# Performance work log

Measured on AMD Instinct MI355X. Metric: run time of the kernel, lower is better.

## Reference

```python
import jax, jax.numpy as jnp
import numpy as np

SEQ = 64  # hard-coded by tf.tile multiples=[1, 64, 1]


def setup_inputs() -> dict:
    key = jax.random.key(0)
    k1, k2, k3, k4 = jax.random.split(key, 4)
    B, V, D = 1024, 300, 512
    return {
        "word_ids_en": jax.random.randint(k1, (B, SEQ), 0, V, dtype=jnp.int32),
        "word_ids_fr": jax.random.randint(k2, (B, SEQ), 0, V, dtype=jnp.int32),
        "emb_kernel": jax.random.normal(k3, (V, D), dtype=jnp.float32) * 0.05,
        "Qdense": jax.random.normal(k4, (D, D), dtype=jnp.float32) * 0.05,
    }


def reference(word_ids_en, word_ids_fr, emb_kernel, Qdense):
    # Encoder side (French)
    embedded_fr = emb_kernel[word_ids_fr]                      # [B, S, D]
    mask_fr = (word_ids_fr != 0).astype(jnp.float32)           # [B, S]
    # Q = K = V = x @ W (same weight, three identical projections in source)
    qkv = jnp.einsum('bsd,de->bse', embedded_fr, Qdense)       # [B, S, D]
    # scores = Q K^T, masked multiplicatively along the key axis (no softmax)
    scores = jnp.einsum('bqd,bkd->bqk', qkv, qkv) * mask_fr[:, None, :]  # [B, S, S]
    encoded = jnp.einsum('bqk,bkd->bqd', scores, qkv)          # [B, S, D]
    # Decoder side (English) + residual add
    embedded_en = emb_kernel[word_ids_en]                      # [B, S, D]
    return embedded_en + encoded
```

## Files before the change

### kernel.cpp

```cpp
#include <hip/hip_runtime.h>
#include <hip/hip_bf16.h>

#define SEQ 64
#define DIM 512
#define VOCAB 300
#define LDQ 516
#define LDSC 72

typedef __attribute__((ext_vector_type(8))) short short8;
typedef __attribute__((ext_vector_type(4))) float floatx4;

static __device__ inline unsigned short f2bf(float x) {
    __hip_bfloat16 t = __float2bfloat16(x);
    return *reinterpret_cast<unsigned short*>(&t);
}

static __device__ inline short8 ld8(const unsigned short* p) {
    union { short8 s; uint2 u[2]; } r;
    r.u[0] = *(const uint2*)p;
    r.u[1] = *(const uint2*)(p + 4);
    return r.s;
}

__global__ __launch_bounds__(64) void proj_kernel(
    const float* __restrict__ emb,
    const float* __restrict__ Q,
    __hip_bfloat16* __restrict__ P)
{
    const int lane = threadIdx.x & 63;
    const int quad = lane >> 4;
    const int l16 = lane & 15;
    const int nt = blockIdx.x;
    const int mt = blockIdx.y;
    const int n = nt * 16 + l16;
    const int vrow = mt * 16 + l16;

    floatx4 acc = {};
#pragma unroll 4
    for (int k0 = 0; k0 < DIM; k0 += 32) {
        float4 x0 = {0, 0, 0, 0}, x1 = {0, 0, 0, 0};
        if (vrow < VOCAB) {
            x0 = *(const float4*)(emb + (size_t)vrow * DIM + k0 + quad * 8);
            x1 = *(const float4*)(emb + (size_t)vrow * DIM + k0 + quad * 8 + 4);
        }
        union { short8 s; unsigned short h[8]; } ua;
        ua.h[0] = f2bf(x0.x); ua.h[1] = f2bf(x0.y); ua.h[2] = f2bf(x0.z); ua.h[3] = f2bf(x0.w);
        ua.h[4] = f2bf(x1.x); ua.h[5] = f2bf(x1.y); ua.h[6] = f2bf(x1.z); ua.h[7] = f2bf(x1.w);

        union { short8 s; unsigned short h[8]; } ub;
#pragma unroll
        for (int j = 0; j < 8; j++)
            ub.h[j] = f2bf(Q[(size_t)(k0 + quad * 8 + j) * DIM + n]);

        acc = __builtin_amdgcn_mfma_f32_16x16x32_bf16(ua.s, ub.s, acc, 0, 0, 0);
    }
#pragma unroll
    for (int r = 0; r < 4; r++) {
        int v = mt * 16 + quad * 4 + r;
        if (v < VOCAB) P[(size_t)v * DIM + n] = __float2bfloat16(acc[r]);
    }
}

__global__ __launch_bounds__(512, 4) void fused_attn_kernel(
    const int* __restrict__ ids_en,
    const int* __restrict__ ids_fr,
    const float* __restrict__ emb,
    const __hip_bfloat16* __restrict__ P,
    float* __restrict__ out)
{
    __shared__ __align__(16) unsigned short qk[SEQ * LDQ];
    __shared__ __align__(16) unsigned short sc[SEQ * LDSC];

    const int b = blockIdx.x;
    const int tid = threadIdx.x;
    const int lane = tid & 63;
    const int w = tid >> 6;
    const int quad = lane >> 4;
    const int l16 = lane & 15;
    const int wv = __builtin_amdgcn_readfirstlane(w);

    {
        int rid[8];
#pragma unroll
        for (int i = 0; i < 8; i++)
            rid[i] = ids_fr[b * SEQ + i * 8 + wv];
        uint4 v[8];
#pragma unroll
        for (int i = 0; i < 8; i++)
            v[i] = *(const uint4*)(P + (size_t)rid[i] * DIM + lane * 8);
#pragma unroll
        for (int i = 0; i < 8; i++) {
            unsigned short* dst = qk + (i * 8 + wv) * LDQ + lane * 8;
            *(uint2*)dst = make_uint2(v[i].x, v[i].y);
            *(uint2*)(dst + 4) = make_uint2(v[i].z, v[i].w);
        }
    }

    const int t0 = w * 2;
    const int qi = w >> 1;
    const int ki0 = t0 & 3, ki1 = (t0 + 1) & 3;
    float mk0 = (ids_fr[b * SEQ + ki0 * 16 + l16] != 0) ? 1.0f : 0.0f;
    float mk1 = (ids_fr[b * SEQ + ki1 * 16 + l16] != 0) ? 1.0f : 0.0f;
    int idE[4];
#pragma unroll
    for (int q = 0; q < 4; q++)
        idE[q] = ids_en[b * SEQ + q * 16 + l16];

    __syncthreads();

    short8 bbr[2][4];
    {
        floatx4 accS[2] = {};
        for (int k0 = 0; k0 < DIM; k0 += 32) {
            short8 aa = ld8(qk + (qi * 16 + l16) * LDQ + k0 + quad * 8);
            short8 b0 = ld8(qk + (ki0 * 16 + l16) * LDQ + k0 + quad * 8);
            accS[0] = __builtin_amdgcn_mfma_f32_16x16x32_bf16(aa, b0, accS[0], 0, 0, 0);
            short8 b1 = ld8(qk + (ki1 * 16 + l16) * LDQ + k0 + quad * 8);
            accS[1] = __builtin_amdgcn_mfma_f32_16x16x32_bf16(aa, b1, accS[1], 0, 0, 0);
        }

#pragma unroll
        for (int kx = 0; kx < 2; kx++)
#pragma unroll
            for (int ni = 0; ni < 4; ni++)
#pragma unroll
                for (int j = 0; j < 8; j++)
                    ((unsigned short*)&bbr[kx][ni])[j] =
                        qk[(kx * 32 + quad * 8 + j) * LDQ + w * 64 + ni * 16 + l16];

#pragma unroll
        for (int r = 0; r < 4; r++) {
            int row = qi * 16 + quad * 4 + r;
            sc[row * LDSC + ki0 * 16 + l16] = f2bf(accS[0][r] * mk0);
            sc[row * LDSC + ki1 * 16 + l16] = f2bf(accS[1][r] * mk1);
        }
    }
    __syncthreads();

    const size_t out_base = (size_t)b * SEQ * DIM;
#pragma unroll
    for (int p = 0; p < 2; p++) {
        floatx4 acc[2][4] = {};
#pragma unroll
        for (int kx = 0; kx < 2; kx++) {
            short8 bf_[2];
#pragma unroll
            for (int mi = 0; mi < 2; mi++)
                bf_[mi] = *(const short8*)(
                    sc + (p * 32 + mi * 16 + l16) * LDSC + kx * 32 + quad * 8);
#pragma unroll
            for (int ni = 0; ni < 4; ni++)
#pragma unroll
                for (int mi = 0; mi < 2; mi++)
                    acc[mi][ni] = __builtin_amdgcn_mfma_f32_16x16x32_bf16(
                        bbr[kx][ni], bf_[mi], acc[mi][ni], 0, 0, 0);
        }

#pragma unroll
        for (int mi = 0; mi < 2; mi++) {
            int m = p * 32 + mi * 16 + l16;
            floatx4 e[4];
#pragma unroll
            for (int ni = 0; ni < 4; ni++)
                e[ni] = *(const floatx4*)(
                    emb + (size_t)idE[p * 2 + mi] * DIM + w * 64 + ni * 16 + quad * 4);
#pragma unroll
            for (int ni = 0; ni < 4; ni++) {
                floatx4 o = e[ni] + acc[mi][ni];
                *(floatx4*)(out + out_base + (size_t)m * DIM + w * 64 + ni * 16 + quad * 4) = o;
            }
        }
    }
}

extern "C" void kernel_launch(void* const* d_in, const int* in_sizes, int n_in,
                              void* d_out, int out_size, void* d_ws, size_t ws_size,
                              hipStream_t stream) {
    const int* ids_en = (const int*)d_in[0];
    const int* ids_fr = (const int*)d_in[1];
    const float* emb  = (const float*)d_in[2];
    const float* Qd   = (const float*)d_in[3];
    float* out = (float*)d_out;

    const int B = in_sizes[0] / SEQ;

    __hip_bfloat16* P = (__hip_bfloat16*)d_ws;

    proj_kernel<<<dim3(32, 19), 64, 0, stream>>>(emb, Qd, P);
    fused_attn_kernel<<<B, 512, 0, stream>>>(ids_en, ids_fr, emb, P, out);
}
```

Measured before the change: 181.3 us.

## Stage output through LDS for coalesced stores; use direct global-to-LDS gather

The gather of projected rows into LDS now uses global_load_lds (direct global-to-LDS DMA) instead of going through registers. The output GEMM operands are swapped so each wave's accumulator tile is written into the reused qk LDS buffer as fp32. The tile is then re-read row-contiguously, the embedding residual is added, and full rows are written with nontemporal stores. This aims to make the global writes and the emb reads fully coalesced, at the cost of extra LDS traffic and added __syncthreads barriers per output pass.

```diff
diff --git a/kernel.cpp b/kernel.cpp
--- a/kernel.cpp
+++ b/kernel.cpp
@@ -20,6 +20,12 @@
     r.u[0] = *(const uint2*)p;
     r.u[1] = *(const uint2*)(p + 4);
     return r.s;
+}
+
+static __device__ inline void gload_lds16(const void* g, void* l) {
+    __builtin_amdgcn_global_load_lds(
+        (const __attribute__((address_space(1))) void*)g,
+        (__attribute__((address_space(3))) void*)l, 16, 0, 0);
 }
 
 __global__ __launch_bounds__(64) void proj_kernel(
@@ -70,6 +76,7 @@
 {
     __shared__ __align__(16) unsigned short qk[SEQ * LDQ];
     __shared__ __align__(16) unsigned short sc[SEQ * LDSC];
+    __shared__ int idsEl[SEQ];
 
     const int b = blockIdx.x;
     const int tid = threadIdx.x;
@@ -77,23 +84,15 @@
     const int w = tid >> 6;
     const int quad = lane >> 4;
     const int l16 = lane & 15;
+    const int n_base = w * 64;
     const int wv = __builtin_amdgcn_readfirstlane(w);
 
-    {
-        int rid[8];
+    if (tid < SEQ) idsEl[tid] = ids_en[b * SEQ + tid];
+
 #pragma unroll
-        for (int i = 0; i < 8; i++)
-            rid[i] = ids_fr[b * SEQ + i * 8 + wv];
-        uint4 v[8];
-#pragma unroll
-        for (int i = 0; i < 8; i++)
-            v[i] = *(const uint4*)(P + (size_t)rid[i] * DIM + lane * 8);
-#pragma unroll
-        for (int i = 0; i < 8; i++) {
-            unsigned short* dst = qk + (i * 8 + wv) * LDQ + lane * 8;
-            *(uint2*)dst = make_uint2(v[i].x, v[i].y);
-            *(uint2*)(dst + 4) = make_uint2(v[i].z, v[i].w);
-        }
+    for (int i = 0; i < 8; i++) {
+        int rid = ids_fr[b * SEQ + i * 8 + wv];
+        gload_lds16(P + (size_t)rid * DIM + lane * 8, qk + (i * 8 + wv) * LDQ);
     }
 
     const int t0 = w * 2;
@@ -101,10 +100,6 @@
     const int ki0 = t0 & 3, ki1 = (t0 + 1) & 3;
     float mk0 = (ids_fr[b * SEQ + ki0 * 16 + l16] != 0) ? 1.0f : 0.0f;
     float mk1 = (ids_fr[b * SEQ + ki1 * 16 + l16] != 0) ? 1.0f : 0.0f;
-    int idE[4];
-#pragma unroll
-    for (int q = 0; q < 4; q++)
-        idE[q] = ids_en[b * SEQ + q * 16 + l16];
 
     __syncthreads();
 
@@ -126,7 +121,7 @@
 #pragma unroll
                 for (int j = 0; j < 8; j++)
                     ((unsigned short*)&bbr[kx][ni])[j] =
-                        qk[(kx * 32 + quad * 8 + j) * LDQ + w * 64 + ni * 16 + l16];
+                        qk[(kx * 32 + quad * 8 + j) * LDQ + n_base + ni * 16 + l16];
 
 #pragma unroll
         for (int r = 0; r < 4; r++) {
@@ -137,38 +132,48 @@
     }
     __syncthreads();
 
+    float* const qf = (float*)qk;
     const size_t out_base = (size_t)b * SEQ * DIM;
 #pragma unroll
     for (int p = 0; p < 2; p++) {
         floatx4 acc[2][4] = {};
 #pragma unroll
         for (int kx = 0; kx < 2; kx++) {
-            short8 bf_[2];
+            short8 af[2];
 #pragma unroll
             for (int mi = 0; mi < 2; mi++)
-                bf_[mi] = *(const short8*)(
-                    sc + (p * 32 + mi * 16 + l16) * LDSC + kx * 32 + quad * 8);
+                af[mi] = *(const short8*)(sc + ((p * 2 + mi) * 16 + l16) * LDSC + kx * 32 + quad * 8);
 #pragma unroll
             for (int ni = 0; ni < 4; ni++)
 #pragma unroll
                 for (int mi = 0; mi < 2; mi++)
                     acc[mi][ni] = __builtin_amdgcn_mfma_f32_16x16x32_bf16(
-                        bbr[kx][ni], bf_[mi], acc[mi][ni], 0, 0, 0);
+                        af[mi], bbr[kx][ni], acc[mi][ni], 0, 0, 0);
         }
 
+        if (p == 1) __syncthreads();
+
 #pragma unroll
-        for (int mi = 0; mi < 2; mi++) {
-            int m = p * 32 + mi * 16 + l16;
-            floatx4 e[4];
-#pragma unroll
-            for (int ni = 0; ni < 4; ni++)
-                e[ni] = *(const floatx4*)(
-                    emb + (size_t)idE[p * 2 + mi] * DIM + w * 64 + ni * 16 + quad * 4);
+        for (int mi = 0; mi < 2; mi++)
 #pragma unroll
             for (int ni = 0; ni < 4; ni++) {
-                floatx4 o = e[ni] + acc[mi][ni];
-                *(floatx4*)(out + out_base + (size_t)m * DIM + w * 64 + ni * 16 + quad * 4) = o;
+                int col = n_base + ni * 16 + l16;
+#pragma unroll
+                for (int r = 0; r < 4; r++)
+                    qf[(mi * 16 + quad * 4 + r) * 516 + col] = acc[mi][ni][r];
             }
+        __syncthreads();
+
+#pragma unroll
+        for (int j = 0; j < 8; j++) {
+            int f = tid * 4 + j * 2048;
+            int lr = f >> 9;
+            int col = f & 511;
+            int grow = p * 32 + lr;
+            floatx4 v = *(const floatx4*)(qf + lr * 516 + col);
+            floatx4 e = *(const floatx4*)(emb + (size_t)idsEl[grow] * DIM + col);
+            floatx4 o = e + v;
+            __builtin_nontemporal_store(o, (floatx4*)(out + out_base + (size_t)grow * DIM + col));
         }
     }
 }
```

Result: faster. 168.7 us (-6.9%).
